# Kernel optimization log

Measured on AMD Instinct MI355X. Metric: run time of the kernel, lower is better.

Reference implementation:

```python
import jax, jax.numpy as jnp
import numpy as np

IN_F = 4096
OUT_F = 4096
BLOCK = 32            # oft_block_size
NBLK = IN_F // BLOCK  # 128 rotation blocks
GROUP = 8             # AQLM group size
NCB = 1               # num codebooks
CB_SIZE = 65536       # 2**16 codes


def setup_inputs() -> dict:
    key = jax.random.key(0)
    k = jax.random.split(key, 6)
    x = jax.random.normal(k[0], (4, 4096, IN_F), dtype=jnp.float32)
    # unconstrained OFT parameter; skew-symmetrized inside the Cayley transform
    oft_r = jax.random.normal(k[1], (NBLK, BLOCK, BLOCK), dtype=jnp.float32) * 0.01
    codes = jax.random.randint(k[2], (OUT_F, IN_F // GROUP, NCB), 0, CB_SIZE, dtype=jnp.int32)
    codebooks = jax.random.normal(k[3], (NCB, CB_SIZE, GROUP), dtype=jnp.float32) * 0.02
    scales = jax.random.uniform(k[4], (OUT_F, 1), dtype=jnp.float32, minval=0.5, maxval=1.5)
    bias = jax.random.normal(k[5], (OUT_F,), dtype=jnp.float32) * 0.01
    return {"x": x, "oft_r": oft_r, "codes": codes, "codebooks": codebooks,
            "scales": scales, "bias": bias}


def _cayley(oft_r):
    # skew-symmetrize then exact Cayley transform: Q = (I + S)(I - S)^{-1}, orthogonal
    S = 0.5 * (oft_r - jnp.swapaxes(oft_r, -1, -2))  # [NBLK, B, B]
    I = jnp.eye(BLOCK, dtype=oft_r.dtype)
    A = I - S
    Bm = I + S
    # Q = Bm @ inv(A)  <=>  Q^T = solve(A^T, Bm^T)
    Qt = jnp.linalg.solve(jnp.swapaxes(A, -1, -2), jnp.swapaxes(Bm, -1, -2))
    return jnp.swapaxes(Qt, -1, -2)  # [NBLK, B, B]


def _dequant_weight(codes, codebooks, scales):
    # codes: [O, G, K] -> gather per-codebook vectors and sum -> [O, G, gs]
    K = codebooks.shape[0]
    gathered = codebooks[jnp.arange(K)[None, None, :], codes]  # [O, G, K, gs]
    w = gathered.sum(axis=2).reshape(codes.shape[0], -1)       # [O, IN_F]
    return w * scales                                          # row-wise scale


def reference(x, oft_r, codes, codebooks, scales, bias):
    expected_dtype = x.dtype
    x = x.astype(oft_r.dtype)  # cast to adapter dtype
    # block-diagonal orthogonal rotation of the input features
    Q = _cayley(oft_r)  # [NBLK, B, B]
    B_, S_, D_ = x.shape
    xb = x.reshape(B_, S_, NBLK, BLOCK)
    xr = jnp.einsum('bsnj,njk->bsnk', xb, Q).reshape(B_, S_, D_)
    # AQLM dequantized linear
    W = _dequant_weight(codes, codebooks, scales)  # [OUT_F, IN_F]
    out = jnp.einsum('bsd,od->bso', xr, W) + bias
    return out.astype(expected_dtype)
```

## Files before the change

### kernel.cpp

```cpp
#include <hip/hip_runtime.h>
#include <cstdint>
#include <cstddef>

#define IN_F 4096
#define OUT_F 4096
#define MTOT 16384
#define NBLKS 128

typedef __bf16 bf16x8 __attribute__((ext_vector_type(8)));
typedef float f32x4 __attribute__((ext_vector_type(4)));
typedef const __attribute__((address_space(1))) void* gas_cvp;
typedef __attribute__((address_space(3))) void* las_vp;

__device__ __forceinline__ unsigned short f2bf(float f) {
  unsigned u = __builtin_bit_cast(unsigned, f);
  u += 0x7fffu + ((u >> 16) & 1u);
  return (unsigned short)(u >> 16);
}

__global__ void cayley_kernel(const float* __restrict__ R, float* __restrict__ Q) {
  __shared__ float M[32][66];
  const int n = blockIdx.x;
  const int t = threadIdx.x;
  const int i = t >> 5, j = t & 31;
  const float* Rb = R + n * 1024;
  const float s = 0.5f * (Rb[i * 32 + j] - Rb[j * 32 + i]);
  M[i][j]      = (i == j ? 1.0f : 0.0f) - s;
  M[i][32 + j] = (i == j ? 1.0f : 0.0f) + s;
  __syncthreads();
  for (int k = 0; k < 32; ++k) {
    const float pivinv = 1.0f / M[k][k];
    const float fik = M[i][k];
    const float mk1 = M[k][j] * pivinv;
    const float mk2 = M[k][32 + j] * pivinv;
    __syncthreads();
    if (i == k) {
      M[i][j] = mk1;
      M[i][32 + j] = mk2;
    } else {
      M[i][j]      -= fik * mk1;
      M[i][32 + j] -= fik * mk2;
    }
    __syncthreads();
  }
  Q[n * 1024 + i * 32 + j] = M[i][32 + j];
}

__global__ void dequant_kernel(const int* __restrict__ codes,
                               const float* __restrict__ cb,
                               const float* __restrict__ scales,
                               unsigned short* __restrict__ W) {
  const int idx = blockIdx.x * 256 + threadIdx.x;
  const int o = idx >> 9;
  const int code = codes[idx];
  const float s = scales[o];
  const float4* cp = (const float4*)(cb + (size_t)code * 8);
  const float4 a = cp[0], b = cp[1];
  uint4 p;
  p.x = (unsigned)f2bf(a.x * s) | ((unsigned)f2bf(a.y * s) << 16);
  p.y = (unsigned)f2bf(a.z * s) | ((unsigned)f2bf(a.w * s) << 16);
  p.z = (unsigned)f2bf(b.x * s) | ((unsigned)f2bf(b.y * s) << 16);
  p.w = (unsigned)f2bf(b.z * s) | ((unsigned)f2bf(b.w * s) << 16);
  ((uint4*)W)[idx] = p;
}

__global__ __launch_bounds__(256) void rotate_kernel(
    const float* __restrict__ x, const float* __restrict__ Q,
    unsigned short* __restrict__ xr) {
  __shared__ float Qs[1024];
  const int n = blockIdx.y;
  const int t = threadIdx.x;
#pragma unroll
  for (int i = 0; i < 4; ++i) Qs[t + i * 256] = Q[n * 1024 + t + i * 256];
  __syncthreads();
  const long m = (long)blockIdx.x * 256 + t;
  const float4* xp = (const float4*)(x + m * IN_F + n * 32);
  float4 xv[8];
#pragma unroll
  for (int j4 = 0; j4 < 8; ++j4) xv[j4] = xp[j4];
  float4 acc[8] = {};
  const float* xs = (const float*)xv;
#pragma unroll
  for (int j = 0; j < 32; ++j) {
    const float xj = xs[j];
#pragma unroll
    for (int c4 = 0; c4 < 8; ++c4) {
      const float4 q = ((const float4*)Qs)[j * 8 + c4];
      acc[c4].x += xj * q.x;
      acc[c4].y += xj * q.y;
      acc[c4].z += xj * q.z;
      acc[c4].w += xj * q.w;
    }
  }
  uint4* op = (uint4*)(xr + m * IN_F + n * 32);
#pragma unroll
  for (int g = 0; g < 4; ++g) {
    const float4 a = acc[2 * g], b = acc[2 * g + 1];
    uint4 p;
    p.x = (unsigned)f2bf(a.x) | ((unsigned)f2bf(a.y) << 16);
    p.y = (unsigned)f2bf(a.z) | ((unsigned)f2bf(a.w) << 16);
    p.z = (unsigned)f2bf(b.x) | ((unsigned)f2bf(b.y) << 16);
    p.w = (unsigned)f2bf(b.z) | ((unsigned)f2bf(b.w) << 16);
    op[g] = p;
  }
}

#define G_BM 256
#define G_BN 256
#define G_BK 32
#define G_KT 128

__global__ __launch_bounds__(512, 2) void gemm_kernel(
    const __bf16* __restrict__ A, const __bf16* __restrict__ B,
    const float* __restrict__ bias, float* __restrict__ C) {
  __shared__ __attribute__((aligned(16))) __bf16 As[4][G_BM * G_BK];
  __shared__ __attribute__((aligned(16))) __bf16 Bs[4][G_BN * G_BK];

  const int t = threadIdx.x;
  const int l = t & 63;
  const int w = t >> 6;
  const int wm = w >> 2;
  const int wn = w & 3;
  const int lr = l & 15;
  const int kg = l >> 4;

  const int bid = blockIdx.x;
  const int wg = (bid & 7) * 128 + (bid >> 3);
  const int bx = wg & 15;
  const int by = wg >> 4;
  const long m0 = (long)by * G_BM;
  const long n0 = (long)bx * G_BN;

  const __bf16* Abase = A + m0 * IN_F;
  const __bf16* Bbase = B + n0 * IN_F;

  int goff[2], soff[2];
#pragma unroll
  for (int q = 0; q < 2; ++q) {
    const int ri = w * 2 + q;
    const int s = ri * 64 + l;
    const int row = s >> 2;
    const int jj = s & 3;
    const int csrc = jj ^ ((row >> 1) & 3);
    goff[q] = row * IN_F + csrc * 8;
    soff[q] = ri * 512;
  }

  const int chunk = kg ^ ((lr >> 1) & 3);
  int aoff[8], boff[4];
#pragma unroll
  for (int i = 0; i < 8; ++i) aoff[i] = (wm * 128 + i * 16 + lr) * G_BK + chunk * 8;
#pragma unroll
  for (int j = 0; j < 4; ++j) boff[j] = (wn * 64 + j * 16 + lr) * G_BK + chunk * 8;

  f32x4 acc[8][4] = {};

#define STAGE(buf, kt) do {                                                   \
    const __bf16* Ak_ = Abase + (kt) * G_BK;                                  \
    const __bf16* Bk_ = Bbase + (kt) * G_BK;                                  \
    _Pragma("unroll")                                                         \
    for (int q_ = 0; q_ < 2; ++q_) {                                          \
      __builtin_amdgcn_global_load_lds((gas_cvp)(Ak_ + goff[q_]),             \
                                       (las_vp)(&As[(buf)][0] + soff[q_]), 16, 0, 0); \
      __builtin_amdgcn_global_load_lds((gas_cvp)(Bk_ + goff[q_]),             \
                                       (las_vp)(&Bs[(buf)][0] + soff[q_]), 16, 0, 0); \
    }                                                                         \
  } while (0)

#define COMPUTE(buf) do {                                                     \
    bf16x8 af_[8], bf_[4];                                                    \
    _Pragma("unroll")                                                         \
    for (int i_ = 0; i_ < 8; ++i_)                                            \
      af_[i_] = *(const bf16x8*)(&As[(buf)][0] + aoff[i_]);                   \
    _Pragma("unroll")                                                         \
    for (int j_ = 0; j_ < 4; ++j_)                                            \
      bf_[j_] = *(const bf16x8*)(&Bs[(buf)][0] + boff[j_]);                   \
    __builtin_amdgcn_s_setprio(1);                                            \
    _Pragma("unroll")                                                         \
    for (int i_ = 0; i_ < 8; ++i_)                                            \
      _Pragma("unroll")                                                       \
      for (int j_ = 0; j_ < 4; ++j_)                                          \
        acc[i_][j_] = __builtin_amdgcn_mfma_f32_16x16x32_bf16(                \
            af_[i_], bf_[j_], acc[i_][j_], 0, 0, 0);                          \
    __builtin_amdgcn_s_setprio(0);                                            \
  } while (0)

#define TILE_SYNC(n) do {                                                     \
    asm volatile("s_waitcnt vmcnt(" #n ")" ::: "memory");                     \
    __builtin_amdgcn_s_barrier();                                             \
    asm volatile("" ::: "memory");                                            \
  } while (0)

  STAGE(0, 0);
  STAGE(1, 1);
  STAGE(2, 2);
  TILE_SYNC(8);

#pragma unroll 4
  for (int kt = 0; kt < G_KT - 4; ++kt) {
    STAGE((kt + 3) & 3, kt + 3);
    COMPUTE(kt & 3);
    TILE_SYNC(8);
  }
  STAGE(3, 127);
  COMPUTE(0);
  TILE_SYNC(8);
  COMPUTE(1);
  TILE_SYNC(4);
  COMPUTE(2);
  TILE_SYNC(0);
  COMPUTE(3);

#undef STAGE
#undef COMPUTE
#undef TILE_SYNC

#pragma unroll
  for (int j = 0; j < 4; ++j) {
    const long gn = n0 + wn * 64 + j * 16 + lr;
    const float bv = bias[gn];
#pragma unroll
    for (int i = 0; i < 8; ++i) {
      const long gm = m0 + wm * 128 + i * 16 + kg * 4;
#pragma unroll
      for (int r = 0; r < 4; ++r) {
        C[(gm + r) * (long)OUT_F + gn] = acc[i][j][r] + bv;
      }
    }
  }
}

extern "C" void kernel_launch(void* const* d_in, const int* in_sizes, int n_in,
                              void* d_out, int out_size, void* d_ws, size_t ws_size,
                              hipStream_t stream) {
  const float* x         = (const float*)d_in[0];
  const float* oft_r     = (const float*)d_in[1];
  const int*   codes     = (const int*)d_in[2];
  const float* codebooks = (const float*)d_in[3];
  const float* scales    = (const float*)d_in[4];
  const float* bias      = (const float*)d_in[5];
  float* out = (float*)d_out;

  char* ws = (char*)d_ws;
  float* Q = (float*)ws;
  unsigned short* XR = (unsigned short*)(ws + (1 << 19));
  unsigned short* W  = (unsigned short*)(ws + (1 << 19) + (size_t)MTOT * IN_F * 2);

  cayley_kernel<<<NBLKS, 1024, 0, stream>>>(oft_r, Q);
  dequant_kernel<<<(OUT_F * (IN_F / 8)) / 256, 256, 0, stream>>>(codes, codebooks, scales, W);
  rotate_kernel<<<dim3(MTOT / 256, NBLKS), 256, 0, stream>>>(x, Q, XR);
  gemm_kernel<<<dim3((MTOT / G_BM) * (OUT_F / G_BN)), 512, 0, stream>>>(
      (const __bf16*)XR, (const __bf16*)W, bias, out);
}
```

Measured before the change: 1.168 ms.

## Fold block rotation into dequantized weights and re-pipeline GEMM LDS loads

Applies the block-diagonal Cayley rotation to the dequantized weight (W·Q^T per 32-column block) instead of to the activations. The rotation work then scales with OUT_F instead of the batch·sequence dimension, and the activation path becomes a plain fp32→bf16 conversion. The GEMM main loop is also restructured: the A fragment loads are split into two halves, and the A and B global→LDS staging is interleaved with the two MFMA halves using extra barriers and sched_barriers. Rounding the rotated weight to bf16 changes numerics slightly, and the added barriers may cost some throughput.

```diff
diff --git a/kernel.cpp b/kernel.cpp
--- a/kernel.cpp
+++ b/kernel.cpp
@@ -46,63 +46,68 @@
   Q[n * 1024 + i * 32 + j] = M[i][32 + j];
 }
 
-__global__ void dequant_kernel(const int* __restrict__ codes,
-                               const float* __restrict__ cb,
-                               const float* __restrict__ scales,
-                               unsigned short* __restrict__ W) {
-  const int idx = blockIdx.x * 256 + threadIdx.x;
-  const int o = idx >> 9;
-  const int code = codes[idx];
-  const float s = scales[o];
-  const float4* cp = (const float4*)(cb + (size_t)code * 8);
-  const float4 a = cp[0], b = cp[1];
-  uint4 p;
-  p.x = (unsigned)f2bf(a.x * s) | ((unsigned)f2bf(a.y * s) << 16);
-  p.y = (unsigned)f2bf(a.z * s) | ((unsigned)f2bf(a.w * s) << 16);
-  p.z = (unsigned)f2bf(b.x * s) | ((unsigned)f2bf(b.y * s) << 16);
-  p.w = (unsigned)f2bf(b.z * s) | ((unsigned)f2bf(b.w * s) << 16);
-  ((uint4*)W)[idx] = p;
-}
-
-__global__ __launch_bounds__(256) void rotate_kernel(
-    const float* __restrict__ x, const float* __restrict__ Q,
-    unsigned short* __restrict__ xr) {
+__global__ __launch_bounds__(256) void dequant_rotw_kernel(
+    const int* __restrict__ codes, const float* __restrict__ cb,
+    const float* __restrict__ scales, const float* __restrict__ Q,
+    unsigned short* __restrict__ W2) {
   __shared__ float Qs[1024];
   const int n = blockIdx.y;
   const int t = threadIdx.x;
 #pragma unroll
   for (int i = 0; i < 4; ++i) Qs[t + i * 256] = Q[n * 1024 + t + i * 256];
   __syncthreads();
-  const long m = (long)blockIdx.x * 256 + t;
-  const float4* xp = (const float4*)(x + m * IN_F + n * 32);
-  float4 xv[8];
-#pragma unroll
-  for (int j4 = 0; j4 < 8; ++j4) xv[j4] = xp[j4];
-  float4 acc[8] = {};
-  const float* xs = (const float*)xv;
-#pragma unroll
-  for (int j = 0; j < 32; ++j) {
-    const float xj = xs[j];
-#pragma unroll
-    for (int c4 = 0; c4 < 8; ++c4) {
-      const float4 q = ((const float4*)Qs)[j * 8 + c4];
-      acc[c4].x += xj * q.x;
-      acc[c4].y += xj * q.y;
-      acc[c4].z += xj * q.z;
-      acc[c4].w += xj * q.w;
+  const int o = blockIdx.x * 256 + t;
+  const float s = scales[o];
+  float wv[32];
+#pragma unroll
+  for (int g = 0; g < 4; ++g) {
+    const int code = codes[o * 512 + n * 4 + g];
+    const float4* cp = (const float4*)(cb + (size_t)code * 8);
+    const float4 a = cp[0], b = cp[1];
+    wv[g * 8 + 0] = a.x * s; wv[g * 8 + 1] = a.y * s;
+    wv[g * 8 + 2] = a.z * s; wv[g * 8 + 3] = a.w * s;
+    wv[g * 8 + 4] = b.x * s; wv[g * 8 + 5] = b.y * s;
+    wv[g * 8 + 6] = b.z * s; wv[g * 8 + 7] = b.w * s;
+  }
+  unsigned po[16];
+#pragma unroll
+  for (int jp = 0; jp < 16; ++jp) {
+    float r[2];
+#pragma unroll
+    for (int h = 0; h < 2; ++h) {
+      const int j = jp * 2 + h;
+      float a = 0.0f;
+#pragma unroll
+      for (int c4 = 0; c4 < 8; ++c4) {
+        const float4 q = ((const float4*)Qs)[j * 8 + c4];
+        a += q.x * wv[c4 * 4 + 0] + q.y * wv[c4 * 4 + 1] +
+             q.z * wv[c4 * 4 + 2] + q.w * wv[c4 * 4 + 3];
+      }
+      r[h] = a;
     }
-  }
-  uint4* op = (uint4*)(xr + m * IN_F + n * 32);
+    po[jp] = (unsigned)f2bf(r[0]) | ((unsigned)f2bf(r[1]) << 16);
+  }
+  uint4* op = (uint4*)(W2 + (size_t)o * IN_F + n * 32);
 #pragma unroll
   for (int g = 0; g < 4; ++g) {
-    const float4 a = acc[2 * g], b = acc[2 * g + 1];
     uint4 p;
-    p.x = (unsigned)f2bf(a.x) | ((unsigned)f2bf(a.y) << 16);
-    p.y = (unsigned)f2bf(a.z) | ((unsigned)f2bf(a.w) << 16);
-    p.z = (unsigned)f2bf(b.x) | ((unsigned)f2bf(b.y) << 16);
-    p.w = (unsigned)f2bf(b.z) | ((unsigned)f2bf(b.w) << 16);
+    p.x = po[g * 4 + 0]; p.y = po[g * 4 + 1];
+    p.z = po[g * 4 + 2]; p.w = po[g * 4 + 3];
     op[g] = p;
   }
+}
+
+__global__ __launch_bounds__(256) void cvt_kernel(
+    const float* __restrict__ x, unsigned short* __restrict__ xc) {
+  const size_t i = (size_t)blockIdx.x * 256 + threadIdx.x;
+  const float4* xp = (const float4*)x + i * 2;
+  const float4 a = xp[0], b = xp[1];
+  uint4 p;
+  p.x = (unsigned)f2bf(a.x) | ((unsigned)f2bf(a.y) << 16);
+  p.y = (unsigned)f2bf(a.z) | ((unsigned)f2bf(a.w) << 16);
+  p.z = (unsigned)f2bf(b.x) | ((unsigned)f2bf(b.y) << 16);
+  p.w = (unsigned)f2bf(b.z) | ((unsigned)f2bf(b.w) << 16);
+  ((uint4*)xc)[i] = p;
 }
 
 #define G_BM 256
@@ -114,7 +119,7 @@
     const __bf16* __restrict__ A, const __bf16* __restrict__ B,
     const float* __restrict__ bias, float* __restrict__ C) {
   __shared__ __attribute__((aligned(16))) __bf16 As[4][G_BM * G_BK];
-  __shared__ __attribute__((aligned(16))) __bf16 Bs[4][G_BN * G_BK];
+  __shared__ __attribute__((aligned(16))) __bf16 Bs[4][G_BM * G_BK];
 
   const int t = threadIdx.x;
   const int l = t & 63;
@@ -155,65 +160,82 @@
 
   f32x4 acc[8][4] = {};
 
-#define STAGE(buf, kt) do {                                                   \
+#define STAGE_A(buf, kt) do {                                                 \
     const __bf16* Ak_ = Abase + (kt) * G_BK;                                  \
-    const __bf16* Bk_ = Bbase + (kt) * G_BK;                                  \
-    _Pragma("unroll")                                                         \
-    for (int q_ = 0; q_ < 2; ++q_) {                                          \
+    _Pragma("unroll")                                                         \
+    for (int q_ = 0; q_ < 2; ++q_)                                            \
       __builtin_amdgcn_global_load_lds((gas_cvp)(Ak_ + goff[q_]),             \
                                        (las_vp)(&As[(buf)][0] + soff[q_]), 16, 0, 0); \
+  } while (0)
+
+#define STAGE_B(buf, kt) do {                                                 \
+    const __bf16* Bk_ = Bbase + (kt) * G_BK;                                  \
+    _Pragma("unroll")                                                         \
+    for (int q_ = 0; q_ < 2; ++q_)                                            \
       __builtin_amdgcn_global_load_lds((gas_cvp)(Bk_ + goff[q_]),             \
                                        (las_vp)(&Bs[(buf)][0] + soff[q_]), 16, 0, 0); \
-    }                                                                         \
   } while (0)
 
-#define COMPUTE(buf) do {                                                     \
-    bf16x8 af_[8], bf_[4];                                                    \
-    _Pragma("unroll")                                                         \
-    for (int i_ = 0; i_ < 8; ++i_)                                            \
-      af_[i_] = *(const bf16x8*)(&As[(buf)][0] + aoff[i_]);                   \
+#define VM_WAIT(n) asm volatile("s_waitcnt vmcnt(" #n ")" ::: "memory")
+
+#define TILE(buf, skt, dostage, vmstmt) do {                                  \
+    bf16x8 a0_[4], a1_[4], b_[4];                                             \
+                                                       \
     _Pragma("unroll")                                                         \
     for (int j_ = 0; j_ < 4; ++j_)                                            \
-      bf_[j_] = *(const bf16x8*)(&Bs[(buf)][0] + boff[j_]);                   \
+      b_[j_] = *(const bf16x8*)(&Bs[(buf)][0] + boff[j_]);                    \
+    _Pragma("unroll")                                                         \
+    for (int i_ = 0; i_ < 4; ++i_)                                            \
+      a0_[i_] = *(const bf16x8*)(&As[(buf)][0] + aoff[i_]);                   \
+    if (dostage) STAGE_A((skt) & 3, skt);                                     \
+    __builtin_amdgcn_s_barrier();                                             \
+    __builtin_amdgcn_sched_barrier(0);                                        \
     __builtin_amdgcn_s_setprio(1);                                            \
     _Pragma("unroll")                                                         \
-    for (int i_ = 0; i_ < 8; ++i_)                                            \
+    for (int i_ = 0; i_ < 4; ++i_)                                            \
       _Pragma("unroll")                                                       \
       for (int j_ = 0; j_ < 4; ++j_)                                          \
         acc[i_][j_] = __builtin_amdgcn_mfma_f32_16x16x32_bf16(                \
-            af_[i_], bf_[j_], acc[i_][j_], 0, 0, 0);                          \
+            a0_[i_], b_[j_], acc[i_][j_], 0, 0, 0);                           \
     __builtin_amdgcn_s_setprio(0);                                            \
+    __builtin_amdgcn_s_barrier();                                             \
+                                                       \
+    _Pragma("unroll")                                                         \
+    for (int i_ = 0; i_ < 4; ++i_)                                            \
+      a1_[i_] = *(const bf16x8*)(&As[(buf)][0] + aoff[4 + i_]);               \
+    if (dostage) STAGE_B((skt) & 3, skt);                                     \
+    vmstmt;                                                                   \
+    __builtin_amdgcn_s_barrier();                                             \
+    __builtin_amdgcn_sched_barrier(0);                                        \
+    __builtin_amdgcn_s_setprio(1);                                            \
+    _Pragma("unroll")                                                         \
+    for (int i_ = 0; i_ < 4; ++i_)                                            \
+      _Pragma("unroll")                                                       \
+      for (int j_ = 0; j_ < 4; ++j_)                                          \
+        acc[4 + i_][j_] = __builtin_amdgcn_mfma_f32_16x16x32_bf16(            \
+            a1_[i_], b_[j_], acc[4 + i_][j_], 0, 0, 0);                       \
+    __builtin_amdgcn_s_setprio(0);                                            \
+    __builtin_amdgcn_s_barrier();                                             \
   } while (0)
 
-#define TILE_SYNC(n) do {                                                     \
-    asm volatile("s_waitcnt vmcnt(" #n ")" ::: "memory");                     \
-    __builtin_amdgcn_s_barrier();                                             \
-    asm volatile("" ::: "memory");                                            \
-  } while (0)
-
-  STAGE(0, 0);
-  STAGE(1, 1);
-  STAGE(2, 2);
-  TILE_SYNC(8);
+  STAGE_A(0, 0); STAGE_B(0, 0);
+  STAGE_A(1, 1); STAGE_B(1, 1);
+  STAGE_A(2, 2); STAGE_B(2, 2);
+  VM_WAIT(8);
+  __builtin_amdgcn_s_barrier();
 
 #pragma unroll 4
-  for (int kt = 0; kt < G_KT - 4; ++kt) {
-    STAGE((kt + 3) & 3, kt + 3);
-    COMPUTE(kt & 3);
-    TILE_SYNC(8);
-  }
-  STAGE(3, 127);
-  COMPUTE(0);
-  TILE_SYNC(8);
-  COMPUTE(1);
-  TILE_SYNC(4);
-  COMPUTE(2);
-  TILE_SYNC(0);
-  COMPUTE(3);
-
-#undef STAGE
-#undef COMPUTE
-#undef TILE_SYNC
+  for (int kt = 0; kt < G_KT - 4; ++kt)
+    TILE(kt & 3, kt + 3, 1, VM_WAIT(8));
+  TILE(0, 127, 1, VM_WAIT(8));
+  TILE(1, 0, 0, VM_WAIT(4));
+  TILE(2, 0, 0, VM_WAIT(0));
+  TILE(3, 0, 0, (void)0);
+
+#undef STAGE_A
+#undef STAGE_B
+#undef VM_WAIT
+#undef TILE
 
 #pragma unroll
   for (int j = 0; j < 4; ++j) {
@@ -243,12 +265,13 @@
 
   char* ws = (char*)d_ws;
   float* Q = (float*)ws;
-  unsigned short* XR = (unsigned short*)(ws + (1 << 19));
-  unsigned short* W  = (unsigned short*)(ws + (1 << 19) + (size_t)MTOT * IN_F * 2);
+  unsigned short* XC = (unsigned short*)(ws + (1 << 19));
+  unsigned short* W2 = (unsigned short*)(ws + (1 << 19) + (size_t)MTOT * IN_F * 2);
 
   cayley_kernel<<<NBLKS, 1024, 0, stream>>>(oft_r, Q);
-  dequant_kernel<<<(OUT_F * (IN_F / 8)) / 256, 256, 0, stream>>>(codes, codebooks, scales, W);
-  rotate_kernel<<<dim3(MTOT / 256, NBLKS), 256, 0, stream>>>(x, Q, XR);
+  dequant_rotw_kernel<<<dim3(OUT_F / 256, NBLKS), 256, 0, stream>>>(
+      codes, codebooks, scales, Q, W2);
+  cvt_kernel<<<(MTOT * (size_t)IN_F) / (256 * 8), 256, 0, stream>>>(x, XC);
   gemm_kernel<<<dim3((MTOT / G_BM) * (OUT_F / G_BN)), 512, 0, stream>>>(
-      (const __bf16*)XR, (const __bf16*)W, bias, out);
-}
+      (const __bf16*)XC, (const __bf16*)W2, bias, out);
+}
```

Measured after the change: 1.064 ms. 1.1x faster.
